# Performance work log

Hardware: AMD Instinct MI355X
Metric: run time of the kernel (lower is better)

The kernel has to match this reference:

```python
import jax, jax.numpy as jnp
import numpy as np

EMBED = 1024
HEADS = 16
HEAD_DIM = EMBED // HEADS
LN_EPS = 1e-5


def _layer_norm(x, g, b):
    m = jnp.mean(x, axis=-1, keepdims=True)
    v = jnp.mean((x - m) ** 2, axis=-1, keepdims=True)
    return (x - m) / jnp.sqrt(v + LN_EPS) * g + b


def _rope(x):
    # x: (b, H, n, D); standard rotary: freqs repeated (cat(freqs, freqs)), rotate_half
    D = x.shape[-1]
    n = x.shape[2]
    inv_freq = 1.0 / (10000.0 ** (jnp.arange(0, D, 2, dtype=jnp.float32) / D))
    freqs = jnp.arange(n, dtype=jnp.float32)[:, None] * inv_freq[None, :]  # (n, D/2)
    emb = jnp.concatenate([freqs, freqs], axis=-1)  # (n, D)
    cos, sin = jnp.cos(emb), jnp.sin(emb)
    rot = jnp.concatenate([-x[..., D // 2:], x[..., : D // 2]], axis=-1)
    return x * cos + rot * sin


def setup_inputs() -> dict:
    key = jax.random.key(0)
    ks = jax.random.split(key, 8)
    E = EMBED
    s_in = 1.0 / np.sqrt(E)
    return {
        "x": jax.random.normal(ks[0], (2, 2048, E), dtype=jnp.float32),
        "in_proj_w": jax.random.uniform(ks[1], (3 * E, E), jnp.float32, -s_in, s_in),
        "in_proj_b": jnp.zeros((3 * E,), jnp.float32),
        "out_proj_w": jax.random.uniform(ks[2], (E, E), jnp.float32, -s_in, s_in),
        "out_proj_b": jnp.zeros((E,), jnp.float32),
        "geglu_w": jax.random.uniform(ks[3], (2 * E, E), jnp.float32, -s_in, s_in),
        "geglu_b": jnp.zeros((2 * E,), jnp.float32),
        "ln1_g": jnp.ones((E,), jnp.float32),
        "ln1_b": jnp.zeros((E,), jnp.float32),
        "ln2_g": jnp.ones((E,), jnp.float32),
        "ln2_b": jnp.zeros((E,), jnp.float32),
    }


def reference(x, in_proj_w, in_proj_b, out_proj_w, out_proj_b,
              geglu_w, geglu_b, ln1_g, ln1_b, ln2_g, ln2_b):
    b, n, E = x.shape
    H, D = HEADS, HEAD_DIM

    # RoPE applied to raw x (q = k = v = x in the module)
    xh = x.reshape(b, n, H, D).transpose(0, 2, 1, 3)  # (b,H,n,D)
    qr = _rope(xh)
    kr = qr  # q and k are identical pre-projection
    q = qr.transpose(0, 2, 1, 3).reshape(b, n, E)
    k = kr.transpose(0, 2, 1, 3).reshape(b, n, E)
    v = x

    # MultiheadAttention (batch-first semantics): in-proj, per-head SDPA, out-proj
    w_q, w_k, w_v = jnp.split(in_proj_w, 3, axis=0)
    b_q, b_k, b_v = jnp.split(in_proj_b, 3, axis=0)
    qp = (q @ w_q.T + b_q).reshape(b, n, H, D).transpose(0, 2, 1, 3)
    kp = (k @ w_k.T + b_k).reshape(b, n, H, D).transpose(0, 2, 1, 3)
    vp = (v @ w_v.T + b_v).reshape(b, n, H, D).transpose(0, 2, 1, 3)
    scores = jnp.einsum("bhqd,bhkd->bhqk", qp, kp) / jnp.sqrt(jnp.float32(D))
    attn = jax.nn.softmax(scores, axis=-1)
    ctx = jnp.einsum("bhqk,bhkd->bhqd", attn, vp)
    ctx = ctx.transpose(0, 2, 1, 3).reshape(b, n, E)
    attn_out = ctx @ out_proj_w.T + out_proj_b

    # residual + LN1
    h = _layer_norm(x + attn_out, ln1_g, ln1_b)

    # GeGLU: Linear(E -> 2E), chunk, value * gelu(gate) (exact erf gelu like torch)
    proj = h @ geglu_w.T + geglu_b
    val, gate = jnp.split(proj, 2, axis=-1)
    fc_out = val * jax.nn.gelu(gate, approximate=False)

    # residual + LN2
    return _layer_norm(h + fc_out, ln2_g, ln2_b)
```

## Files before the change

### kernel.cpp

```cpp
#include <hip/hip_runtime.h>


typedef __bf16 bf16;
typedef bf16 bf16x8 __attribute__((ext_vector_type(8)));
typedef bf16 bf16x4 __attribute__((ext_vector_type(4)));
typedef float f32x4 __attribute__((ext_vector_type(4)));

#define EMB 1024
#define SEQ 2048
#define NTOK 4096
#define NH 16
#define HD 64

__device__ __forceinline__ f32x4 mfma16(bf16x8 a, bf16x8 b, f32x4 c) {
  return __builtin_amdgcn_mfma_f32_16x16x32_bf16(a, b, c, 0, 0, 0);
}

__device__ __forceinline__ void gll16(const void* g, void* l) {
  __builtin_amdgcn_global_load_lds(
      (const __attribute__((address_space(1))) void*)g,
      (__attribute__((address_space(3))) void*)l, 16, 0, 0);
}


__global__ __launch_bounds__(256) void rope_cast(
    const float* __restrict__ x, bf16* __restrict__ xb, bf16* __restrict__ qr) {
  int idx = blockIdx.x * 256 + threadIdx.x;
  int row = idx >> 9;
  int i = idx & 511;
  int h = i >> 5, d2 = i & 31;
  int pos = row & (SEQ - 1);
  int c0 = h * HD + d2;
  size_t base = (size_t)row * EMB;
  float x0 = x[base + c0], x1 = x[base + c0 + 32];
  float invf = exp2f(-(float)d2 * 0.4152410118609203f);
  float ang = (float)pos * invf;
  float sn, cs;
  sincosf(ang, &sn, &cs);
  qr[base + c0] = (bf16)(x0 * cs - x1 * sn);
  qr[base + c0 + 32] = (bf16)(x1 * cs + x0 * sn);
  xb[base + c0] = (bf16)x0;
  xb[base + c0 + 32] = (bf16)x1;
}

__global__ __launch_bounds__(256) void cast_w(
    const float* __restrict__ w, bf16* __restrict__ o, int n) {
  int i = (blockIdx.x * 256 + threadIdx.x) * 4;
  if (i < n) {
    float4 f = *(const float4*)(w + i);
    o[i] = (bf16)f.x; o[i + 1] = (bf16)f.y;
    o[i + 2] = (bf16)f.z; o[i + 3] = (bf16)f.w;
  }
}

__global__ __launch_bounds__(256) void gemm_in(
    const bf16* __restrict__ Aq, const bf16* __restrict__ Ax,
    const bf16* __restrict__ W, const float* __restrict__ bias,
    bf16* __restrict__ qk, bf16* __restrict__ vT) {
  __shared__ bf16 As[128 * 32];
  __shared__ bf16 Bs[128 * 32];
  const int tid = threadIdx.x, lane = tid & 63, wave = tid >> 6;
  const int quad = lane >> 4, l16 = lane & 15;
  const int m0 = blockIdx.y * 128, n0 = blockIdx.x * 128;
  const bf16* A = (n0 < 2048) ? Aq : Ax;
  const int K = 1024;
  const int wm = (wave >> 1) * 64, wn = (wave & 1) * 64;
  const int srow = wave * 32 + (lane >> 2);
  const int scol = (lane & 3) * 8;
  f32x4 acc[4][4] = {};
  for (int k0 = 0; k0 < K; k0 += 32) {
    __syncthreads();
    gll16(A + (size_t)(m0 + srow) * K + k0 + scol, As + wave * 1024);
    gll16(A + (size_t)(m0 + srow + 16) * K + k0 + scol, As + wave * 1024 + 512);
    gll16(W + (size_t)(n0 + srow) * K + k0 + scol, Bs + wave * 1024);
    gll16(W + (size_t)(n0 + srow + 16) * K + k0 + scol, Bs + wave * 1024 + 512);
    __syncthreads();
    bf16x8 af[4], bw[4];
#pragma unroll
    for (int t = 0; t < 4; ++t) {
      af[t] = *(const bf16x8*)(As + (wm + t * 16 + l16) * 32 + quad * 8);
      bw[t] = *(const bf16x8*)(Bs + (wn + t * 16 + l16) * 32 + quad * 8);
    }
#pragma unroll
    for (int mt = 0; mt < 4; ++mt)
#pragma unroll
      for (int nt = 0; nt < 4; ++nt)
        acc[mt][nt] = mfma16(af[mt], bw[nt], acc[mt][nt]);
  }
  if (n0 < 2048) {
#pragma unroll
    for (int mt = 0; mt < 4; ++mt)
      for (int nt = 0; nt < 4; ++nt) {
        const int n = n0 + wn + nt * 16 + l16;
        const float bv = bias[n];
#pragma unroll
        for (int r = 0; r < 4; ++r) {
          const int m = m0 + wm + mt * 16 + quad * 4 + r;
          qk[(size_t)m * 2048 + n] = (bf16)(acc[mt][nt][r] + bv);
        }
      }
  } else {
#pragma unroll
    for (int mt = 0; mt < 4; ++mt)
      for (int nt = 0; nt < 4; ++nt) {
        const int n = n0 + wn + nt * 16 + l16;
        const float bv = bias[n];
        const int m = m0 + wm + mt * 16 + quad * 4;
        const int bb = m >> 11, s = m & 2047;
        bf16x4 pk;
#pragma unroll
        for (int r = 0; r < 4; ++r) pk[r] = (bf16)(acc[mt][nt][r] + bv);
        *(bf16x4*)(vT + (((size_t)bb * 1024 + (n - 2048)) << 11) + s) = pk;
      }
  }
}

__global__ __launch_bounds__(256) void gemm_bt(
    const bf16* __restrict__ A, const bf16* __restrict__ W,
    const float* __restrict__ bias,
    float* __restrict__ outF, bf16* __restrict__ outB,
    int M, int N, int K) {
  __shared__ bf16 As[128 * 32];
  __shared__ bf16 Bs[128 * 32];
  const int tid = threadIdx.x, lane = tid & 63, wave = tid >> 6;
  const int quad = lane >> 4, l16 = lane & 15;
  const int m0 = blockIdx.y * 128, n0 = blockIdx.x * 128;
  const int wm = (wave >> 1) * 64, wn = (wave & 1) * 64;
  const int srow = wave * 32 + (lane >> 2);
  const int scol = (lane & 3) * 8;
  f32x4 acc[4][4] = {};
  for (int k0 = 0; k0 < K; k0 += 32) {
    __syncthreads();
    gll16(A + (size_t)(m0 + srow) * K + k0 + scol, As + wave * 1024);
    gll16(A + (size_t)(m0 + srow + 16) * K + k0 + scol, As + wave * 1024 + 512);
    gll16(W + (size_t)(n0 + srow) * K + k0 + scol, Bs + wave * 1024);
    gll16(W + (size_t)(n0 + srow + 16) * K + k0 + scol, Bs + wave * 1024 + 512);
    __syncthreads();
    bf16x8 af[4], bw[4];
#pragma unroll
    for (int t = 0; t < 4; ++t) {
      af[t] = *(const bf16x8*)(As + (wm + t * 16 + l16) * 32 + quad * 8);
      bw[t] = *(const bf16x8*)(Bs + (wn + t * 16 + l16) * 32 + quad * 8);
    }
#pragma unroll
    for (int mt = 0; mt < 4; ++mt)
#pragma unroll
      for (int nt = 0; nt < 4; ++nt)
        acc[mt][nt] = mfma16(af[mt], bw[nt], acc[mt][nt]);
  }
#pragma unroll
  for (int mt = 0; mt < 4; ++mt)
    for (int nt = 0; nt < 4; ++nt) {
      const int n = n0 + wn + nt * 16 + l16;
      const float bv = bias ? bias[n] : 0.0f;
#pragma unroll
      for (int r = 0; r < 4; ++r) {
        const int m = m0 + wm + mt * 16 + quad * 4 + r;
        const float v = acc[mt][nt][r] + bv;
        if (outF) outF[(size_t)m * N + n] = v;
        if (outB) outB[(size_t)m * N + n] = (bf16)v;
      }
    }
}

__global__ __launch_bounds__(256) void gemm_bt64(
    const bf16* __restrict__ A, const bf16* __restrict__ W,
    const float* __restrict__ bias, float* __restrict__ outF,
    int M, int N, int K) {
  __shared__ bf16 As[128 * 32];
  __shared__ bf16 Bs[64 * 32];
  const int tid = threadIdx.x, lane = tid & 63, wave = tid >> 6;
  const int quad = lane >> 4, l16 = lane & 15;
  const int m0 = blockIdx.y * 128, n0 = blockIdx.x * 64;
  const int wm = (wave >> 1) * 64, wn = (wave & 1) * 32;
  const int srow = wave * 32 + (lane >> 2);
  const int srowB = wave * 16 + (lane >> 2);
  const int scol = (lane & 3) * 8;
  f32x4 acc[4][2] = {};
  for (int k0 = 0; k0 < K; k0 += 32) {
    __syncthreads();
    gll16(A + (size_t)(m0 + srow) * K + k0 + scol, As + wave * 1024);
    gll16(A + (size_t)(m0 + srow + 16) * K + k0 + scol, As + wave * 1024 + 512);
    gll16(W + (size_t)(n0 + srowB) * K + k0 + scol, Bs + wave * 512);
    __syncthreads();
    bf16x8 af[4], bw[2];
#pragma unroll
    for (int t = 0; t < 4; ++t)
      af[t] = *(const bf16x8*)(As + (wm + t * 16 + l16) * 32 + quad * 8);
#pragma unroll
    for (int t = 0; t < 2; ++t)
      bw[t] = *(const bf16x8*)(Bs + (wn + t * 16 + l16) * 32 + quad * 8);
#pragma unroll
    for (int mt = 0; mt < 4; ++mt)
#pragma unroll
      for (int nt = 0; nt < 2; ++nt)
        acc[mt][nt] = mfma16(af[mt], bw[nt], acc[mt][nt]);
  }
#pragma unroll
  for (int mt = 0; mt < 4; ++mt)
    for (int nt = 0; nt < 2; ++nt) {
      const int n = n0 + wn + nt * 16 + l16;
      const float bv = bias[n];
#pragma unroll
      for (int r = 0; r < 4; ++r) {
        const int m = m0 + wm + mt * 16 + quad * 4 + r;
        outF[(size_t)m * N + n] = acc[mt][nt][r] + bv;
      }
    }
}

__global__ __launch_bounds__(256) void attn3(
    const bf16* __restrict__ QK, const bf16* __restrict__ VT,
    bf16* __restrict__ ctx) {
  __shared__ __align__(16) bf16 Ks[64 * 64];
  __shared__ __align__(16) bf16 Vs[64 * 64];
  __shared__ __align__(16) bf16 Ps[4 * 16 * 64];
  const int tid = threadIdx.x, lane = tid & 63, wave = tid >> 6;
  const int quad = lane >> 4, l16 = lane & 15;
  const int qt = blockIdx.x, h = blockIdx.y, b = blockIdx.z;

  bf16x8 qf[2];
  {
    const int qrow = qt * 64 + wave * 16 + l16;
    const bf16* qp = QK + (size_t)(b * SEQ + qrow) * 2048 + h * HD + quad * 8;
#pragma unroll
    for (int kt = 0; kt < 2; ++kt) {
      bf16x8 t = *(const bf16x8*)(qp + kt * 32);
#pragma unroll
      for (int j = 0; j < 8; ++j) t[j] = (bf16)((float)t[j] * 0.125f);
      qf[kt] = t;
    }
  }
  bf16x8 ones;
#pragma unroll
  for (int j = 0; j < 8; ++j) ones[j] = (bf16)1.0f;
  f32x4 o[4] = {};
  f32x4 l = {};

  const int srow = tid >> 3;
  const int sc = tid & 7;
  const bf16* kg = QK + (size_t)(b * SEQ) * 2048 + 1024 + h * HD + sc * 8;
  const bf16* vg = VT + ((size_t)(b * NH + h) * HD) * SEQ + sc * 8;
  bf16* pb = Ps + wave * 1024;

  for (int kb = 0; kb < SEQ; kb += 64) {
    __syncthreads();
#pragma unroll
    for (int p = 0; p < 2; ++p) {
      const int row = p * 32 + srow;
      const int sw = (sc ^ (row & 7)) * 8;
      bf16x8 kv = *(const bf16x8*)(kg + (size_t)(kb + row) * 2048);
      *(bf16x8*)(Ks + row * 64 + sw) = kv;
      bf16x8 vv = *(const bf16x8*)(vg + (size_t)row * SEQ + kb);
      *(bf16x8*)(Vs + row * 64 + sw) = vv;
    }
    __syncthreads();
    f32x4 s[4] = {};
#pragma unroll
    for (int kc = 0; kc < 4; ++kc) {
      const int krow = kc * 16 + l16;
#pragma unroll
      for (int kt = 0; kt < 2; ++kt) {
        bf16x8 kf = *(const bf16x8*)(
            Ks + krow * 64 + (((kt * 4 + quad) ^ (l16 & 7)) * 8));
        s[kc] = mfma16(qf[kt], kf, s[kc]);
      }
    }
#pragma unroll
    for (int kc = 0; kc < 4; ++kc)
#pragma unroll
      for (int r = 0; r < 4; ++r) {
        const int row = quad * 4 + r;
        pb[row * 64 + (((kc * 2 + (l16 >> 3)) ^ (row & 7)) * 8) + (l16 & 7)] =
            (bf16)__expf(s[kc][r]);
      }
#pragma unroll
    for (int kt = 0; kt < 2; ++kt) {
      bf16x8 pf = *(const bf16x8*)(
          pb + l16 * 64 + (((kt * 4 + quad) ^ (l16 & 7)) * 8));
      l = mfma16(pf, ones, l);
#pragma unroll
      for (int dc = 0; dc < 4; ++dc) {
        bf16x8 vf = *(const bf16x8*)(
            Vs + (dc * 16 + l16) * 64 + (((kt * 4 + quad) ^ (l16 & 7)) * 8));
        o[dc] = mfma16(pf, vf, o[dc]);
      }
    }
  }
#pragma unroll
  for (int dc = 0; dc < 4; ++dc)
#pragma unroll
    for (int r = 0; r < 4; ++r) {
      const int qrow = qt * 64 + wave * 16 + quad * 4 + r;
      ctx[(size_t)(b * SEQ + qrow) * EMB + h * HD + dc * 16 + l16] =
          (bf16)(o[dc][r] / l[r]);
    }
}

__global__ __launch_bounds__(256) void ln1_k(
    const float* __restrict__ x, const float* __restrict__ ao,
    const float* __restrict__ g, const float* __restrict__ bta,
    float* __restrict__ hF, bf16* __restrict__ hB) {
  int row = blockIdx.x, tid = threadIdx.x;
  const float* xr = x + (size_t)row * EMB;
  const float* ar = ao + (size_t)row * EMB;
  float v[4], s = 0.0f, s2 = 0.0f;
#pragma unroll
  for (int i = 0; i < 4; ++i) {
    float t = xr[tid + i * 256] + ar[tid + i * 256];
    v[i] = t; s += t; s2 += t * t;
  }
#pragma unroll
  for (int off = 1; off < 64; off <<= 1) {
    s += __shfl_xor(s, off, 64);
    s2 += __shfl_xor(s2, off, 64);
  }
  __shared__ float red[8];
  int wave = tid >> 6, lane = tid & 63;
  if (lane == 0) { red[wave] = s; red[4 + wave] = s2; }
  __syncthreads();
  s = red[0] + red[1] + red[2] + red[3];
  s2 = red[4] + red[5] + red[6] + red[7];
  float mean = s * (1.0f / EMB);
  float var = s2 * (1.0f / EMB) - mean * mean;
  float inv = rsqrtf(var + 1e-5f);
#pragma unroll
  for (int i = 0; i < 4; ++i) {
    int c = tid + i * 256;
    float t = (v[i] - mean) * inv * g[c] + bta[c];
    hF[(size_t)row * EMB + c] = t;
    hB[(size_t)row * EMB + c] = (bf16)t;
  }
}

__global__ __launch_bounds__(256) void geglu_ln2(
    const float* __restrict__ h, const bf16* __restrict__ proj,
    const float* __restrict__ g, const float* __restrict__ bta,
    float* __restrict__ out) {
  int row = blockIdx.x, tid = threadIdx.x;
  const float* hr = h + (size_t)row * EMB;
  const bf16* pr = proj + (size_t)row * 2048;
  float v[4], s = 0.0f, s2 = 0.0f;
#pragma unroll
  for (int i = 0; i < 4; ++i) {
    int c = tid + i * 256;
    float val = (float)pr[c];
    float gate = (float)pr[1024 + c];
    float ge = 0.5f * gate * (1.0f + erff(gate * 0.70710678f));
    float t = hr[c] + val * ge;
    v[i] = t; s += t; s2 += t * t;
  }
#pragma unroll
  for (int off = 1; off < 64; off <<= 1) {
    s += __shfl_xor(s, off, 64);
    s2 += __shfl_xor(s2, off, 64);
  }
  __shared__ float red[8];
  int wave = tid >> 6, lane = tid & 63;
  if (lane == 0) { red[wave] = s; red[4 + wave] = s2; }
  __syncthreads();
  s = red[0] + red[1] + red[2] + red[3];
  s2 = red[4] + red[5] + red[6] + red[7];
  float mean = s * (1.0f / EMB);
  float var = s2 * (1.0f / EMB) - mean * mean;
  float inv = rsqrtf(var + 1e-5f);
#pragma unroll
  for (int i = 0; i < 4; ++i) {
    int c = tid + i * 256;
    out[(size_t)row * EMB + c] = (v[i] - mean) * inv * g[c] + bta[c];
  }
}

extern "C" void kernel_launch(void* const* d_in, const int* in_sizes, int n_in,
                              void* d_out, int out_size, void* d_ws, size_t ws_size,
                              hipStream_t stream) {
  const float* x = (const float*)d_in[0];
  const float* inW = (const float*)d_in[1];
  const float* inB = (const float*)d_in[2];
  const float* outW = (const float*)d_in[3];
  const float* opB = (const float*)d_in[4];
  const float* ggW = (const float*)d_in[5];
  const float* ggB = (const float*)d_in[6];
  const float* g1 = (const float*)d_in[7];
  const float* b1 = (const float*)d_in[8];
  const float* g2 = (const float*)d_in[9];
  const float* b2 = (const float*)d_in[10];
  float* out = (float*)d_out;
  char* ws = (char*)d_ws;
  const size_t MB = 1ull << 20;
  bf16* xb = (bf16*)(ws);
  bf16* qr = (bf16*)(ws + 8 * MB);
  bf16* ctx = (bf16*)(ws + 8 * MB);
  bf16* wI = (bf16*)(ws + 16 * MB);
  bf16* wO = (bf16*)(ws + 22 * MB);
  bf16* wG = (bf16*)(ws + 24 * MB);
  bf16* qk = (bf16*)(ws + 28 * MB);
  bf16* projB = (bf16*)(ws + 28 * MB);
  bf16* vbT = (bf16*)(ws + 44 * MB);
  float* ao = (float*)(ws + 44 * MB);
  bf16* hB = (bf16*)(ws + 60 * MB);

  rope_cast<<<NTOK * 512 / 256, 256, 0, stream>>>(x, xb, qr);
  cast_w<<<(3072 * 1024 / 4) / 256, 256, 0, stream>>>(inW, wI, 3072 * 1024);
  cast_w<<<(1024 * 1024 / 4) / 256, 256, 0, stream>>>(outW, wO, 1024 * 1024);
  cast_w<<<(2048 * 1024 / 4) / 256, 256, 0, stream>>>(ggW, wG, 2048 * 1024);
  gemm_in<<<dim3(24, 32), 256, 0, stream>>>(qr, xb, wI, inB, qk, vbT);
  attn3<<<dim3(32, 16, 2), 256, 0, stream>>>(qk, vbT, ctx);
  gemm_bt64<<<dim3(16, 32), 256, 0, stream>>>(ctx, wO, opB, ao,
                                              NTOK, 1024, 1024);
  ln1_k<<<NTOK, 256, 0, stream>>>(x, ao, g1, b1, ao, hB);
  gemm_bt<<<dim3(16, 32), 256, 0, stream>>>(hB, wG, ggB, nullptr, projB,
                                            NTOK, 2048, 1024);
  geglu_ln2<<<NTOK, 256, 0, stream>>>(ao, projB, g2, b2, out);
}
```

Before: 282.1 us.

## Rewrite attention with 32x32 MFMA tiles and 128-query blocks

Attention now uses 32x32x16 bf16 MFMA instructions, with each wave handling 32 query rows instead of 16, so each block covers 128 queries. K and V tiles loaded into LDS are therefore reused across twice as many queries, halving global K/V traffic. S is computed transposed (K as A operand), so the exp'd probabilities are written to LDS in the layout the PV MFMA needs. The row sum is accumulated in registers rather than with an extra ones-MFMA. The grid has half as many blocks (512), which lowers occupancy and parallelism, and the larger per-wave accumulators raise register pressure.

Measured after the change: 294.7 us. 4.5% more time.

```diff
diff --git a/kernel.cpp b/kernel.cpp
--- a/kernel.cpp
+++ b/kernel.cpp
@@ -5,6 +5,7 @@
 typedef bf16 bf16x8 __attribute__((ext_vector_type(8)));
 typedef bf16 bf16x4 __attribute__((ext_vector_type(4)));
 typedef float f32x4 __attribute__((ext_vector_type(4)));
+typedef float f32x16 __attribute__((ext_vector_type(16)));
 
 #define EMB 1024
 #define SEQ 2048
@@ -14,6 +15,9 @@
 
 __device__ __forceinline__ f32x4 mfma16(bf16x8 a, bf16x8 b, f32x4 c) {
   return __builtin_amdgcn_mfma_f32_16x16x32_bf16(a, b, c, 0, 0, 0);
+}
+__device__ __forceinline__ f32x16 mfma32(bf16x8 a, bf16x8 b, f32x16 c) {
+  return __builtin_amdgcn_mfma_f32_32x32x16_bf16(a, b, c, 0, 0, 0);
 }
 
 __device__ __forceinline__ void gll16(const void* g, void* l) {
@@ -209,92 +213,92 @@
     }
 }
 
-__global__ __launch_bounds__(256) void attn3(
+__global__ __launch_bounds__(256) void attn4(
     const bf16* __restrict__ QK, const bf16* __restrict__ VT,
     bf16* __restrict__ ctx) {
   __shared__ __align__(16) bf16 Ks[64 * 64];
   __shared__ __align__(16) bf16 Vs[64 * 64];
-  __shared__ __align__(16) bf16 Ps[4 * 16 * 64];
+  __shared__ __align__(16) bf16 Ps[4 * 32 * 64];
+  __shared__ float Linv[4][32];
   const int tid = threadIdx.x, lane = tid & 63, wave = tid >> 6;
-  const int quad = lane >> 4, l16 = lane & 15;
+  const int hi = lane >> 5, l31 = lane & 31, l7 = lane & 7;
   const int qt = blockIdx.x, h = blockIdx.y, b = blockIdx.z;
 
-  bf16x8 qf[2];
+  bf16x8 qf[4];
   {
-    const int qrow = qt * 64 + wave * 16 + l16;
-    const bf16* qp = QK + (size_t)(b * SEQ + qrow) * 2048 + h * HD + quad * 8;
-#pragma unroll
-    for (int kt = 0; kt < 2; ++kt) {
-      bf16x8 t = *(const bf16x8*)(qp + kt * 32);
-#pragma unroll
-      for (int j = 0; j < 8; ++j) t[j] = (bf16)((float)t[j] * 0.125f);
-      qf[kt] = t;
-    }
-  }
-  bf16x8 ones;
-#pragma unroll
-  for (int j = 0; j < 8; ++j) ones[j] = (bf16)1.0f;
-  f32x4 o[4] = {};
-  f32x4 l = {};
-
-  const int srow = tid >> 3;
-  const int sc = tid & 7;
-  const bf16* kg = QK + (size_t)(b * SEQ) * 2048 + 1024 + h * HD + sc * 8;
-  const bf16* vg = VT + ((size_t)(b * NH + h) * HD) * SEQ + sc * 8;
-  bf16* pb = Ps + wave * 1024;
+    const int qrow = qt * 128 + wave * 32 + l31;
+    const bf16* qp = QK + (size_t)(b * SEQ + qrow) * 2048 + h * HD + hi * 8;
+#pragma unroll
+    for (int t = 0; t < 4; ++t) {
+      bf16x8 v = *(const bf16x8*)(qp + t * 16);
+#pragma unroll
+      for (int j = 0; j < 8; ++j) v[j] = (bf16)((float)v[j] * 0.125f);
+      qf[t] = v;
+    }
+  }
+  f32x16 o0 = {}, o1 = {};
+  float lpart = 0.0f;
+
+  const bf16* kg = QK + (size_t)(b * SEQ) * 2048 + 1024 + h * HD;
+  const bf16* vg = VT + ((size_t)(b * NH + h) * HD) * 2048;
+  bf16* pw = Ps + wave * 2048;
 
   for (int kb = 0; kb < SEQ; kb += 64) {
     __syncthreads();
 #pragma unroll
     for (int p = 0; p < 2; ++p) {
-      const int row = p * 32 + srow;
-      const int sw = (sc ^ (row & 7)) * 8;
-      bf16x8 kv = *(const bf16x8*)(kg + (size_t)(kb + row) * 2048);
-      *(bf16x8*)(Ks + row * 64 + sw) = kv;
-      bf16x8 vv = *(const bf16x8*)(vg + (size_t)row * SEQ + kb);
-      *(bf16x8*)(Vs + row * 64 + sw) = vv;
-    }
-    __syncthreads();
-    f32x4 s[4] = {};
-#pragma unroll
-    for (int kc = 0; kc < 4; ++kc) {
-      const int krow = kc * 16 + l16;
-#pragma unroll
-      for (int kt = 0; kt < 2; ++kt) {
-        bf16x8 kf = *(const bf16x8*)(
-            Ks + krow * 64 + (((kt * 4 + quad) ^ (l16 & 7)) * 8));
-        s[kc] = mfma16(qf[kt], kf, s[kc]);
+      const int c = p * 256 + tid;
+      const int row = c >> 3, c16 = c & 7;
+      const int sw = row * 64 + ((c16 ^ (row & 7)) * 8);
+      *(bf16x8*)(Ks + sw) = *(const bf16x8*)(kg + (size_t)(kb + row) * 2048 + c16 * 8);
+      *(bf16x8*)(Vs + sw) = *(const bf16x8*)(vg + (size_t)row * 2048 + kb + c16 * 8);
+    }
+    __syncthreads();
+    f32x16 s0 = {}, s1 = {};
+#pragma unroll
+    for (int t = 0; t < 4; ++t) {
+      const int swc = ((t * 2 + hi) ^ l7) * 8;
+      bf16x8 k0 = *(const bf16x8*)(Ks + l31 * 64 + swc);
+      bf16x8 k1 = *(const bf16x8*)(Ks + (32 + l31) * 64 + swc);
+      s0 = mfma32(k0, qf[t], s0);
+      s1 = mfma32(k1, qf[t], s1);
+    }
+#pragma unroll
+    for (int kc = 0; kc < 2; ++kc) {
+      const f32x16& sv = kc ? s1 : s0;
+#pragma unroll
+      for (int g = 0; g < 4; ++g) {
+        bf16x4 pk;
+#pragma unroll
+        for (int j = 0; j < 4; ++j) {
+          float e = __expf(sv[g * 4 + j]);
+          lpart += e;
+          pk[j] = (bf16)e;
+        }
+        *(bf16x4*)(pw + l31 * 64 + (((kc * 4 + g) ^ l7) * 8) + hi * 4) = pk;
       }
     }
 #pragma unroll
-    for (int kc = 0; kc < 4; ++kc)
-#pragma unroll
-      for (int r = 0; r < 4; ++r) {
-        const int row = quad * 4 + r;
-        pb[row * 64 + (((kc * 2 + (l16 >> 3)) ^ (row & 7)) * 8) + (l16 & 7)] =
-            (bf16)__expf(s[kc][r]);
-      }
-#pragma unroll
-    for (int kt = 0; kt < 2; ++kt) {
-      bf16x8 pf = *(const bf16x8*)(
-          pb + l16 * 64 + (((kt * 4 + quad) ^ (l16 & 7)) * 8));
-      l = mfma16(pf, ones, l);
-#pragma unroll
-      for (int dc = 0; dc < 4; ++dc) {
-        bf16x8 vf = *(const bf16x8*)(
-            Vs + (dc * 16 + l16) * 64 + (((kt * 4 + quad) ^ (l16 & 7)) * 8));
-        o[dc] = mfma16(pf, vf, o[dc]);
-      }
-    }
-  }
-#pragma unroll
-  for (int dc = 0; dc < 4; ++dc)
-#pragma unroll
-    for (int r = 0; r < 4; ++r) {
-      const int qrow = qt * 64 + wave * 16 + quad * 4 + r;
-      ctx[(size_t)(b * SEQ + qrow) * EMB + h * HD + dc * 16 + l16] =
-          (bf16)(o[dc][r] / l[r]);
-    }
+    for (int t2 = 0; t2 < 4; ++t2) {
+      const int swc = ((t2 * 2 + hi) ^ l7) * 8;
+      bf16x8 pf = *(const bf16x8*)(pw + l31 * 64 + swc);
+      bf16x8 v0 = *(const bf16x8*)(Vs + l31 * 64 + swc);
+      bf16x8 v1 = *(const bf16x8*)(Vs + (32 + l31) * 64 + swc);
+      o0 = mfma32(pf, v0, o0);
+      o1 = mfma32(pf, v1, o1);
+    }
+  }
+  float ltot = lpart + __shfl_xor(lpart, 32, 64);
+  if (lane < 32) Linv[wave][lane] = 1.0f / ltot;
+#pragma unroll
+  for (int r = 0; r < 16; ++r) {
+    const int qloc = (r & 3) + 8 * (r >> 2) + 4 * hi;
+    const float inv = Linv[wave][qloc];
+    const int qrow = qt * 128 + wave * 32 + qloc;
+    bf16* cp = ctx + (size_t)(b * SEQ + qrow) * EMB + h * HD;
+    cp[l31] = (bf16)(o0[r] * inv);
+    cp[32 + l31] = (bf16)(o1[r] * inv);
+  }
 }
 
 __global__ __launch_bounds__(256) void ln1_k(
@@ -405,7 +409,7 @@
   cast_w<<<(1024 * 1024 / 4) / 256, 256, 0, stream>>>(outW, wO, 1024 * 1024);
   cast_w<<<(2048 * 1024 / 4) / 256, 256, 0, stream>>>(ggW, wG, 2048 * 1024);
   gemm_in<<<dim3(24, 32), 256, 0, stream>>>(qr, xb, wI, inB, qk, vbT);
-  attn3<<<dim3(32, 16, 2), 256, 0, stream>>>(qk, vbT, ctx);
+  attn4<<<dim3(16, 16, 2), 256, 0, stream>>>(qk, vbT, ctx);
   gemm_bt64<<<dim3(16, 32), 256, 0, stream>>>(ctx, wO, opB, ao,
                                               NTOK, 1024, 1024);
   ln1_k<<<NTOK, 256, 0, stream>>>(x, ao, g1, b1, ao, hB);
```
